# Kernel optimization log

Measured on AMD Instinct MI355X. Metric: run time of the kernel, lower is better.

## Reference

```python
import jax, jax.numpy as jnp
import numpy as np

LORA_SCALING = 16.0 / 8.0  # alpha / r
NUM_HEADS = 12
HEAD_DIM = 64


def lora_linear(x, w, b, lora_a, lora_b):
    # base: x @ w.T + b ; lora: (x @ a.T) @ b_.T * scaling
    base = jnp.einsum('bnd,od->bno', x, w) + b
    low = jnp.einsum('bnd,rd->bnr', x, lora_a)
    return base + jnp.einsum('bnr,or->bno', low, lora_b) * LORA_SCALING


def setup_inputs() -> dict:
    key = jax.random.key(0)
    ks = jax.random.split(key, 9)
    B, N, D, R = 64, 197, 768, 8
    s = lambda k, shape, scale: jax.random.normal(k, shape, jnp.float32) * scale
    return {
        'x': s(ks[0], (B, N, D), 1.0),
        'qkv_w': s(ks[1], (3 * D, D), 0.02),
        'qkv_b': s(ks[2], (3 * D,), 0.02),
        'qkv_lora_a': s(ks[3], (R, D), 0.02),
        'qkv_lora_b': jnp.zeros((3 * D, R), jnp.float32) + s(ks[4], (3 * D, R), 0.02),
        'out_w': s(ks[5], (D, D), 0.02),
        'out_b': s(ks[6], (D,), 0.02),
        'out_lora_a': s(ks[7], (R, D), 0.02),
        'out_lora_b': s(ks[8], (D, R), 0.02),
    }


def reference(x, qkv_w, qkv_b, qkv_lora_a, qkv_lora_b, out_w, out_b, out_lora_a, out_lora_b):
    B, N, D = x.shape
    H, Hd = NUM_HEADS, HEAD_DIM
    qkv = lora_linear(x, qkv_w, qkv_b, qkv_lora_a, qkv_lora_b)  # [B,N,3D]
    qkv = qkv.reshape(B, N, 3, H, Hd).transpose(2, 0, 3, 1, 4)  # [3,B,H,N,Hd]
    q, k, v = qkv[0], qkv[1], qkv[2]
    attn = jnp.einsum('bhnd,bhmd->bhnm', q, k) * (Hd ** -0.5)
    attn = jax.nn.softmax(attn, axis=-1)  # dropout is identity in eval mode
    out = jnp.einsum('bhnm,bhmd->bhnd', attn, v)  # [B,H,N,Hd]
    out = out.transpose(0, 2, 1, 3).reshape(B, N, D)
    return lora_linear(out, out_w, out_b, out_lora_a, out_lora_b)
```

## Files before the change

### kernel.cpp

```cpp
#include <hip/hip_runtime.h>
#include <stdint.h>

typedef __attribute__((ext_vector_type(8))) short short8;
typedef __attribute__((ext_vector_type(4))) float f32x4;

#define SB __builtin_amdgcn_sched_barrier(0)

__device__ __forceinline__ unsigned short f2bf(float f) {
  unsigned u = __float_as_uint(f);
  u += 0x7FFF + ((u >> 16) & 1);
  return (unsigned short)(u >> 16);
}


__global__ __launch_bounds__(256) void k_prep3(const float* __restrict__ x,
                                               const float* __restrict__ qkv_w,
                                               const float* __restrict__ out_w,
                                               const float* __restrict__ qkv_la,
                                               const float* __restrict__ qkv_lb,
                                               const float* __restrict__ out_la,
                                               const float* __restrict__ out_lb,
                                               unsigned short* __restrict__ Apk,
                                               unsigned short* __restrict__ Wq,
                                               unsigned short* __restrict__ Wo,
                                               unsigned short* __restrict__ Vtpk) {
  __shared__ unsigned short xs[16 * 776];
  const int bid = blockIdx.x;
  const int t = threadIdx.x;
  if (bid < 788) {
    const int mt = bid;
    const float4* x4 = (const float4*)(x + (size_t)mt * 16 * 768);
#pragma unroll
    for (int i = 0; i < 12; ++i) {
      float4 v = x4[i * 256 + t];
      int e0 = (i * 256 + t) * 4;
      int row = e0 / 768, col = e0 - row * 768;
      unsigned short* d = &xs[row * 776 + col];
      d[0] = f2bf(v.x); d[1] = f2bf(v.y); d[2] = f2bf(v.z); d[3] = f2bf(v.w);
    }
    __syncthreads();
    const int w = t >> 6, l = t & 63;
    const int lr = l & 15, lg = l >> 4;
#pragma unroll
    for (int kk = 0; kk < 6; ++kk) {
      int kc = w * 6 + kk;
      short8 v = *(const short8*)(&xs[lr * 776 + kc * 32 + lg * 8]);
      *(short8*)(Apk + (size_t)(kc * 788 + mt) * 512 + l * 8) = v;
    }
  } else if (bid < 1940) {
    const bool isq = bid < 1652;
    const float* W = isq ? qkv_w : out_w;
    const float* la = isq ? qkv_la : out_la;
    const float* lb = isq ? qkv_lb : out_lb;
    unsigned short* dst = isq ? Wq : Wo;
    const int NRT = isq ? 144 : 48;
    const int base = isq ? 788 : 1652;
    int wv = ((bid - base) * 256 + t) >> 6;
    int l = t & 63;
    int rt = wv / 24, kc = wv - rt * 24;
    int lr = l & 15, lg = l >> 4;
    const int o = rt * 16 + lr;
    const int d0 = kc * 32 + lg * 8;
    const float* src = W + (size_t)o * 768 + d0;
    float4 a = *(const float4*)src;
    float4 b = *(const float4*)(src + 4);
    float wvv[8] = {a.x, a.y, a.z, a.w, b.x, b.y, b.z, b.w};
    const float4* lb4 = (const float4*)(lb + (size_t)o * 8);
    float4 p0 = lb4[0], p1 = lb4[1];
    float lbv[8] = {p0.x, p0.y, p0.z, p0.w, p1.x, p1.y, p1.z, p1.w};
#pragma unroll
    for (int r = 0; r < 8; ++r) {
      const float4* la4 = (const float4*)(la + (size_t)r * 768 + d0);
      float4 c = la4[0], dd = la4[1];
      float s = 2.0f * lbv[r];
      wvv[0] += s * c.x;  wvv[1] += s * c.y;  wvv[2] += s * c.z;  wvv[3] += s * c.w;
      wvv[4] += s * dd.x; wvv[5] += s * dd.y; wvv[6] += s * dd.z; wvv[7] += s * dd.w;
    }
    short8 oo;
#pragma unroll
    for (int e = 0; e < 8; ++e) oo[e] = f2bf(wvv[e]);
    *(short8*)(dst + (size_t)(kc * NRT + rt) * 512 + l * 8) = oo;
  } else {
    int r = (bid - 1940) * 256 + t;
    int bh = r >> 6, hd = r & 63;
    unsigned short* base = Vtpk + (size_t)bh * 14336 + (24 + (hd >> 4)) * 512;
#pragma unroll
    for (int c = 0; c < 27; ++c) {
      int n = 197 + c;
      base[((hd & 15) + 16 * ((n & 31) >> 3)) * 8 + (n & 7)] = 0;
    }
  }
}

template <int MODE, int NT, int NRTB>
__global__ __launch_bounds__(256, 3) void k_gp4(
    const unsigned short* __restrict__ Apk, const unsigned short* __restrict__ Bpk,
    const float* __restrict__ bias, unsigned short* __restrict__ Qpk,
    unsigned short* __restrict__ Kpk, unsigned short* __restrict__ Vtpk,
    float* __restrict__ outp) {
  __shared__ __align__(16) char bl[49152];
  const int w = threadIdx.x >> 6, l = threadIdx.x & 63;
  const int lr = l & 15, lg = l >> 4;
  const int nwg = gridDim.x;
  const int orig = blockIdx.x;
  const int qq = nwg >> 3, rr = nwg & 7, xcd = orig & 7;
  const int wgid = (xcd < rr ? xcd * (qq + 1) : rr * (qq + 1) + (xcd - rr) * qq) + (orig >> 3);
  const int mg = wgid / NT, nt = wgid - mg * NT;
  int mtw = mg * 4 + w;
  if (mtw > 196) mtw = 196;
  const int m0 = mtw * 64, n0 = nt * 64;

  const size_t KSA = 788 * 512;
  const unsigned short* pa = Apk + (size_t)(mtw * 4) * 512 + l * 8;

  auto* lds3 = (__attribute__((address_space(3))) char*)bl;
  auto STB = [&](int kc) {
    const unsigned short* g = Bpk + ((size_t)kc * NRTB + nt * 4 + w) * 512 + l * 8;
    __builtin_amdgcn_global_load_lds((const __attribute__((address_space(1))) void*)g,
                                     (__attribute__((address_space(3))) void*)(lds3 + ((kc % 12) * 4 + w) * 1024),
                                     16, 0, 0);
  };

  f32x4 acc[4][4];
#pragma unroll
  for (int i = 0; i < 4; ++i)
#pragma unroll
    for (int j = 0; j < 4; ++j) acc[i][j] = (f32x4){0.f, 0.f, 0.f, 0.f};

  short8 ab[2][4];
#define LDA4(dst, kt) \
  { const unsigned short* q_ = pa + (size_t)(kt) * KSA; \
    dst[0] = *(const short8*)(q_); dst[1] = *(const short8*)(q_ + 512); \
    dst[2] = *(const short8*)(q_ + 1024); dst[3] = *(const short8*)(q_ + 1536); }

#pragma unroll
  for (int kc = 0; kc < 12; ++kc) STB(kc);
  asm volatile("s_waitcnt vmcnt(0)" ::: "memory");
  SB;
  __builtin_amdgcn_s_barrier();
  LDA4(ab[0], 0);
  LDA4(ab[1], 1);

#pragma unroll
  for (int kt = 0; kt < 24; ++kt) {
    if (kt == 12) {
      asm volatile("s_waitcnt vmcnt(4)" ::: "memory");
      SB;
      __builtin_amdgcn_s_barrier();
    }
    short8 bfr[4];
    const char* sbase = (const char*)bl + (kt % 12) * 4096;
#pragma unroll
    for (int nf = 0; nf < 4; ++nf)
      bfr[nf] = *(const short8*)(sbase + nf * 1024 + l * 16);
    if (kt == 11) {
      asm volatile("s_waitcnt lgkmcnt(0)" ::: "memory");
      SB;
      __builtin_amdgcn_s_barrier();
#pragma unroll
      for (int kc = 12; kc < 24; ++kc) STB(kc);
    }
    __builtin_amdgcn_s_setprio(1);
#pragma unroll
    for (int mf = 0; mf < 4; ++mf)
#pragma unroll
      for (int nf = 0; nf < 4; ++nf)
        acc[mf][nf] = __builtin_amdgcn_mfma_f32_16x16x32_bf16(ab[kt & 1][mf], bfr[nf], acc[mf][nf], 0, 0, 0);
    __builtin_amdgcn_s_setprio(0);
    if (kt + 2 < 24) LDA4(ab[kt & 1], kt + 2);
  }
#undef LDA4

  float bo[4];
#pragma unroll
  for (int nf = 0; nf < 4; ++nf) bo[nf] = bias[n0 + nf * 16 + lr];
  const int which = nt / 12;
  const int hh = nt - which * 12;
#pragma unroll
  for (int mf = 0; mf < 4; ++mf) {
#pragma unroll
    for (int v = 0; v < 4; ++v) {
      int m = m0 + mf * 16 + lg * 4 + v;
      int b = m / 197;
      int n = m - b * 197;
#pragma unroll
      for (int nf = 0; nf < 4; ++nf) {
        float val = acc[mf][nf][v] + bo[nf];
        if (MODE == 0) {
          int bh = b * 12 + hh;
          unsigned short hv = f2bf(val);
          if (which == 2) {
            Vtpk[(size_t)bh * 14336 + ((n >> 5) * 4 + nf) * 512 +
                 (lr + 16 * ((n & 31) >> 3)) * 8 + (n & 7)] = hv;
          } else {
            unsigned short* dst = (which == 0) ? Qpk : Kpk;
            dst[(size_t)bh * 14336 + ((nf >> 1) * 14 + (n >> 4)) * 512 +
                ((n & 15) + 16 * ((nf & 1) * 2 + (lr >> 3))) * 8 + (lr & 7)] = hv;
          }
        } else {
          outp[(size_t)m * 768 + n0 + nf * 16 + lr] = val;
        }
      }
    }
  }
}

__global__ __launch_bounds__(256) void k_attn_w(const unsigned short* __restrict__ Qpk,
                                                const unsigned short* __restrict__ Kpk,
                                                const unsigned short* __restrict__ Vtpk,
                                                unsigned short* __restrict__ Apk) {
  __shared__ __align__(16) unsigned short Ps[4][7 * 512];
  const int w = threadIdx.x >> 6, l = threadIdx.x & 63;
  const int lr = l & 15, lg = l >> 4;
  const int nwg = gridDim.x;
  const int orig = blockIdx.x;
  const int qq = nwg >> 3, xcd = orig & 7;
  const int wgid = xcd * qq + (orig >> 3);
  const int task = wgid * 4 + w;
  const int bh = task / 13, t = task - bh * 13;
  const int b = bh / 12, h = bh - b * 12;
  const unsigned short* Qb = Qpk + (size_t)bh * 14336;
  const unsigned short* Kb = Kpk + (size_t)bh * 14336;
  const unsigned short* Vb = Vtpk + (size_t)bh * 14336;

  short8 aq0 = *(const short8*)(Qb + (size_t)t * 512 + l * 8);
  short8 aq1 = *(const short8*)(Qb + (size_t)(14 + t) * 512 + l * 8);
  f32x4 s[13];
#pragma unroll
  for (int jt = 0; jt < 13; ++jt) {
    f32x4 a = (f32x4){0.f, 0.f, 0.f, 0.f};
    short8 bk0 = *(const short8*)(Kb + (size_t)jt * 512 + l * 8);
    short8 bk1 = *(const short8*)(Kb + (size_t)(14 + jt) * 512 + l * 8);
    __builtin_amdgcn_s_setprio(1);
    a = __builtin_amdgcn_mfma_f32_16x16x32_bf16(aq0, bk0, a, 0, 0, 0);
    a = __builtin_amdgcn_mfma_f32_16x16x32_bf16(aq1, bk1, a, 0, 0, 0);
    __builtin_amdgcn_s_setprio(0);
    s[jt] = a;
  }
#pragma unroll
  for (int v = 0; v < 4; ++v)
    if (lr >= 5) s[12][v] = -1.0e30f;
  float mx[4] = {-3.0e38f, -3.0e38f, -3.0e38f, -3.0e38f};
#pragma unroll
  for (int jt = 0; jt < 13; ++jt)
#pragma unroll
    for (int v = 0; v < 4; ++v) mx[v] = fmaxf(mx[v], s[jt][v]);
#pragma unroll
  for (int v = 0; v < 4; ++v) {
    mx[v] = fmaxf(mx[v], __shfl_xor(mx[v], 1));
    mx[v] = fmaxf(mx[v], __shfl_xor(mx[v], 2));
    mx[v] = fmaxf(mx[v], __shfl_xor(mx[v], 4));
    mx[v] = fmaxf(mx[v], __shfl_xor(mx[v], 8));
  }
  float sum[4] = {0.f, 0.f, 0.f, 0.f};
  const float cc = 0.125f * 1.44269504088896341f;
#pragma unroll
  for (int jt = 0; jt < 13; ++jt)
#pragma unroll
    for (int v = 0; v < 4; ++v) {
      float pv = exp2f((s[jt][v] - mx[v]) * cc);
      s[jt][v] = pv;
      sum[v] += pv;
    }
#pragma unroll
  for (int v = 0; v < 4; ++v) {
    sum[v] += __shfl_xor(sum[v], 1);
    sum[v] += __shfl_xor(sum[v], 2);
    sum[v] += __shfl_xor(sum[v], 4);
    sum[v] += __shfl_xor(sum[v], 8);
  }
  float inv[4];
#pragma unroll
  for (int v = 0; v < 4; ++v) inv[v] = 1.0f / sum[v];
  unsigned short* pw = &Ps[w][0];
#pragma unroll
  for (int jt = 0; jt < 13; ++jt) {
    const int base = (jt >> 1) * 512 + ((jt & 1) * 2 + (lr >> 3)) * 128 + (lr & 7);
#pragma unroll
    for (int v = 0; v < 4; ++v)
      pw[base + (lg * 4 + v) * 8] = f2bf(s[jt][v] * inv[v]);
  }
  {
    const int base = 6 * 512 + (2 + (lr >> 3)) * 128 + (lr & 7);
#pragma unroll
    for (int v = 0; v < 4; ++v) pw[base + (lg * 4 + v) * 8] = 0;
  }
  f32x4 oacc[4];
#pragma unroll
  for (int jo = 0; jo < 4; ++jo) oacc[jo] = (f32x4){0.f, 0.f, 0.f, 0.f};
#pragma unroll
  for (int kk = 0; kk < 7; ++kk) {
    short8 pa = *(const short8*)(pw + kk * 512 + l * 8);
    __builtin_amdgcn_s_setprio(1);
#pragma unroll
    for (int jo = 0; jo < 4; ++jo) {
      short8 bv = *(const short8*)(Vb + (size_t)(kk * 4 + jo) * 512 + l * 8);
      oacc[jo] = __builtin_amdgcn_mfma_f32_16x16x32_bf16(pa, bv, oacc[jo], 0, 0, 0);
    }
    __builtin_amdgcn_s_setprio(0);
  }
  const int q0 = t * 16;
#pragma unroll
  for (int jo = 0; jo < 4; ++jo) {
    const int kc = h * 2 + (jo >> 1);
    const int lgp = (jo & 1) * 2 + (lr >> 3);
    const int e = lr & 7;
#pragma unroll
    for (int v = 0; v < 4; ++v) {
      int n = q0 + lg * 4 + v;
      if (n < 197) {
        int m = b * 197 + n;
        Apk[((size_t)(kc * 788 + (m >> 4)) * 64 + (m & 15) + 16 * lgp) * 8 + e] = f2bf(oacc[jo][v]);
      }
    }
  }
}

extern "C" void kernel_launch(void* const* d_in, const int* in_sizes, int n_in,
                              void* d_out, int out_size, void* d_ws, size_t ws_size,
                              hipStream_t stream) {
  const float* x      = (const float*)d_in[0];
  const float* qkv_w  = (const float*)d_in[1];
  const float* qkv_b  = (const float*)d_in[2];
  const float* qkv_la = (const float*)d_in[3];
  const float* qkv_lb = (const float*)d_in[4];
  const float* out_w  = (const float*)d_in[5];
  const float* out_b  = (const float*)d_in[6];
  const float* out_la = (const float*)d_in[7];
  const float* out_lb = (const float*)d_in[8];
  float* out = (float*)d_out;

  char* p = (char*)d_ws;
  auto carve = [&](size_t bytes) {
    char* r = p;
    p += (bytes + 255) & ~(size_t)255;
    return r;
  };
  unsigned short* Apk  = (unsigned short*)carve((size_t)788 * 24 * 512 * 2 + 32768);
  unsigned short* Wqpk = (unsigned short*)carve((size_t)144 * 24 * 512 * 2);
  unsigned short* Wopk = (unsigned short*)carve((size_t)48 * 24 * 512 * 2);
  unsigned short* Qpk  = (unsigned short*)carve((size_t)768 * 14336 * 2);
  unsigned short* Kpk  = (unsigned short*)carve((size_t)768 * 14336 * 2);
  unsigned short* Vtpk = (unsigned short*)carve((size_t)768 * 14336 * 2);

  k_prep3<<<2132, 256, 0, stream>>>(x, qkv_w, out_w, qkv_la, qkv_lb, out_la, out_lb,
                                    Apk, Wqpk, Wopk, Vtpk);
  k_gp4<0, 36, 144><<<50 * 36, 256, 0, stream>>>(Apk, Wqpk, qkv_b, Qpk, Kpk, Vtpk, nullptr);
  k_attn_w<<<2496, 256, 0, stream>>>(Qpk, Kpk, Vtpk, Apk);
  k_gp4<1, 12, 48><<<50 * 12, 256, 0, stream>>>(Apk, Wopk, out_b, nullptr, nullptr, nullptr, out);
}
```

Measured before the change: 152.9 us.

## Widen GEMM N tile to 128 with six-stage B pipeline

The projection GEMM kernel now computes a 64x128 tile per wave instead of 64x64. This doubles the MFMA work per A-fragment load and halves global A traffic. B staging in LDS becomes a 6-chunk refill loop, and the epilogue computes head indices per column fragment. The cost is double the accumulator registers, lower occupancy (2 waves per SIMD), and half as many workgroups, which may hurt load balance, especially for the output projection.

Result: no change. 155.5 us (+1.7%).

```diff
diff --git a/kernel.cpp b/kernel.cpp
--- a/kernel.cpp
+++ b/kernel.cpp
@@ -93,7 +93,7 @@
 }
 
 template <int MODE, int NT, int NRTB>
-__global__ __launch_bounds__(256, 3) void k_gp4(
+__global__ __launch_bounds__(256, 2) void k_gp5(
     const unsigned short* __restrict__ Apk, const unsigned short* __restrict__ Bpk,
     const float* __restrict__ bias, unsigned short* __restrict__ Qpk,
     unsigned short* __restrict__ Kpk, unsigned short* __restrict__ Vtpk,
@@ -108,24 +108,29 @@
   const int mg = wgid / NT, nt = wgid - mg * NT;
   int mtw = mg * 4 + w;
   if (mtw > 196) mtw = 196;
-  const int m0 = mtw * 64, n0 = nt * 64;
+  const int m0 = mtw * 64, n0 = nt * 128;
 
   const size_t KSA = 788 * 512;
   const unsigned short* pa = Apk + (size_t)(mtw * 4) * 512 + l * 8;
 
   auto* lds3 = (__attribute__((address_space(3))) char*)bl;
   auto STB = [&](int kc) {
-    const unsigned short* g = Bpk + ((size_t)kc * NRTB + nt * 4 + w) * 512 + l * 8;
-    __builtin_amdgcn_global_load_lds((const __attribute__((address_space(1))) void*)g,
-                                     (__attribute__((address_space(3))) void*)(lds3 + ((kc % 12) * 4 + w) * 1024),
-                                     16, 0, 0);
+    const int s = kc % 6;
+#pragma unroll
+    for (int i = 0; i < 2; ++i) {
+      const int rtl = w * 2 + i;
+      const unsigned short* g = Bpk + ((size_t)kc * NRTB + nt * 8 + rtl) * 512 + l * 8;
+      __builtin_amdgcn_global_load_lds((const __attribute__((address_space(1))) void*)g,
+                                       (__attribute__((address_space(3))) void*)(lds3 + (s * 8 + rtl) * 1024),
+                                       16, 0, 0);
+    }
   };
 
-  f32x4 acc[4][4];
+  f32x4 acc[4][8];
 #pragma unroll
   for (int i = 0; i < 4; ++i)
 #pragma unroll
-    for (int j = 0; j < 4; ++j) acc[i][j] = (f32x4){0.f, 0.f, 0.f, 0.f};
+    for (int j = 0; j < 8; ++j) acc[i][j] = (f32x4){0.f, 0.f, 0.f, 0.f};
 
   short8 ab[2][4];
 #define LDA4(dst, kt) \
@@ -134,7 +139,7 @@
     dst[2] = *(const short8*)(q_ + 1024); dst[3] = *(const short8*)(q_ + 1536); }
 
 #pragma unroll
-  for (int kc = 0; kc < 12; ++kc) STB(kc);
+  for (int kc = 0; kc < 6; ++kc) STB(kc);
   asm volatile("s_waitcnt vmcnt(0)" ::: "memory");
   SB;
   __builtin_amdgcn_s_barrier();
@@ -143,39 +148,47 @@
 
 #pragma unroll
   for (int kt = 0; kt < 24; ++kt) {
-    if (kt == 12) {
+    if (kt != 0 && (kt % 6) == 0) {
       asm volatile("s_waitcnt vmcnt(4)" ::: "memory");
       SB;
       __builtin_amdgcn_s_barrier();
     }
-    short8 bfr[4];
-    const char* sbase = (const char*)bl + (kt % 12) * 4096;
-#pragma unroll
-    for (int nf = 0; nf < 4; ++nf)
+    short8 bfr[8];
+    const char* sbase = (const char*)bl + (kt % 6) * 8192;
+#pragma unroll
+    for (int nf = 0; nf < 8; ++nf)
       bfr[nf] = *(const short8*)(sbase + nf * 1024 + l * 16);
-    if (kt == 11) {
+    if ((kt % 6) == 5 && kt < 23) {
       asm volatile("s_waitcnt lgkmcnt(0)" ::: "memory");
       SB;
       __builtin_amdgcn_s_barrier();
 #pragma unroll
-      for (int kc = 12; kc < 24; ++kc) STB(kc);
+      for (int kc2 = 0; kc2 < 6; ++kc2) STB(kt + 1 + kc2);
     }
     __builtin_amdgcn_s_setprio(1);
 #pragma unroll
     for (int mf = 0; mf < 4; ++mf)
 #pragma unroll
-      for (int nf = 0; nf < 4; ++nf)
+      for (int nf = 0; nf < 8; ++nf)
         acc[mf][nf] = __builtin_amdgcn_mfma_f32_16x16x32_bf16(ab[kt & 1][mf], bfr[nf], acc[mf][nf], 0, 0, 0);
     __builtin_amdgcn_s_setprio(0);
     if (kt + 2 < 24) LDA4(ab[kt & 1], kt + 2);
   }
 #undef LDA4
 
-  float bo[4];
-#pragma unroll
-  for (int nf = 0; nf < 4; ++nf) bo[nf] = bias[n0 + nf * 16 + lr];
-  const int which = nt / 12;
-  const int hh = nt - which * 12;
+  float bo[8];
+  int which[8], hh[8], hd[8];
+#pragma unroll
+  for (int nf = 0; nf < 8; ++nf) {
+    int o = n0 + nf * 16 + lr;
+    bo[nf] = bias[o];
+    if (MODE == 0) {
+      which[nf] = o / 768;
+      int win = o - which[nf] * 768;
+      hh[nf] = win >> 6;
+      hd[nf] = win & 63;
+    }
+  }
 #pragma unroll
   for (int mf = 0; mf < 4; ++mf) {
 #pragma unroll
@@ -184,18 +197,18 @@
       int b = m / 197;
       int n = m - b * 197;
 #pragma unroll
-      for (int nf = 0; nf < 4; ++nf) {
+      for (int nf = 0; nf < 8; ++nf) {
         float val = acc[mf][nf][v] + bo[nf];
         if (MODE == 0) {
-          int bh = b * 12 + hh;
+          int bh = b * 12 + hh[nf];
           unsigned short hv = f2bf(val);
-          if (which == 2) {
-            Vtpk[(size_t)bh * 14336 + ((n >> 5) * 4 + nf) * 512 +
+          if (which[nf] == 2) {
+            Vtpk[(size_t)bh * 14336 + ((n >> 5) * 4 + (hd[nf] >> 4)) * 512 +
                  (lr + 16 * ((n & 31) >> 3)) * 8 + (n & 7)] = hv;
           } else {
-            unsigned short* dst = (which == 0) ? Qpk : Kpk;
-            dst[(size_t)bh * 14336 + ((nf >> 1) * 14 + (n >> 4)) * 512 +
-                ((n & 15) + 16 * ((nf & 1) * 2 + (lr >> 3))) * 8 + (lr & 7)] = hv;
+            unsigned short* dst = (which[nf] == 0) ? Qpk : Kpk;
+            dst[(size_t)bh * 14336 + ((hd[nf] >> 5) * 14 + (n >> 4)) * 512 +
+                ((n & 15) + 16 * ((hd[nf] & 31) >> 3)) * 8 + (hd[nf] & 7)] = hv;
           }
         } else {
           outp[(size_t)m * 768 + n0 + nf * 16 + lr] = val;
@@ -345,7 +358,7 @@
 
   k_prep3<<<2132, 256, 0, stream>>>(x, qkv_w, out_w, qkv_la, qkv_lb, out_la, out_lb,
                                     Apk, Wqpk, Wopk, Vtpk);
-  k_gp4<0, 36, 144><<<50 * 36, 256, 0, stream>>>(Apk, Wqpk, qkv_b, Qpk, Kpk, Vtpk, nullptr);
+  k_gp5<0, 18, 144><<<50 * 18, 256, 0, stream>>>(Apk, Wqpk, qkv_b, Qpk, Kpk, Vtpk, nullptr);
   k_attn_w<<<2496, 256, 0, stream>>>(Qpk, Kpk, Vtpk, Apk);
-  k_gp4<1, 12, 48><<<50 * 12, 256, 0, stream>>>(Apk, Wopk, out_b, nullptr, nullptr, nullptr, out);
-}
+  k_gp5<1, 6, 48><<<50 * 6, 256, 0, stream>>>(Apk, Wopk, out_b, nullptr, nullptr, nullptr, out);
+}
```
